# Performance work log

Measured on AMD Instinct MI355X. Metric: run time of the kernel, lower is better.

The kernel has to match this reference:

```python
import jax, jax.numpy as jnp
import numpy as np

NEG_LARGE = -2.0**32 + 1.0


def setup_inputs() -> dict:
    key = jax.random.key(0)
    ks = jax.random.split(key, 8)
    B, L, D = 2048, 200, 64  # D = embedding_dim, features are 2D wide
    H1, H2 = 80, 40
    queries = jax.random.normal(ks[0], (B, 2 * D), dtype=jnp.float32)
    user_behaviors = jax.random.normal(ks[1], (B, L, 2 * D), dtype=jnp.float32)
    masks = jax.random.randint(ks[2], (B, L), 0, 2, dtype=jnp.int32)
    s = 1.0 / np.sqrt(8 * D)
    w1 = jax.random.uniform(ks[3], (8 * D, H1), minval=-s, maxval=s, dtype=jnp.float32)
    b1 = jnp.zeros((H1,), jnp.float32)
    s2 = 1.0 / np.sqrt(H1)
    w2 = jax.random.uniform(ks[4], (H1, H2), minval=-s2, maxval=s2, dtype=jnp.float32)
    b2 = jnp.zeros((H2,), jnp.float32)
    s3 = 1.0 / np.sqrt(H2)
    w3 = jax.random.uniform(ks[5], (H2, 1), minval=-s3, maxval=s3, dtype=jnp.float32)
    b3 = jnp.zeros((1,), jnp.float32)
    return {"queries": queries, "user_behaviors": user_behaviors, "masks": masks,
            "w1": w1, "b1": b1, "w2": w2, "b2": b2, "w3": w3, "b3": b3}


def reference(queries, user_behaviors, masks, w1, b1, w2, b2, w3, b3):
    B, L, twoD = user_behaviors.shape
    q = jnp.broadcast_to(queries[:, None, :], (B, L, twoD))  # (B, L, 2D)
    feats = jnp.concatenate([q, user_behaviors, q - user_behaviors,
                             q * user_behaviors], axis=-1)  # (B, L, 8D)
    h = jax.nn.sigmoid(jnp.einsum('blf,fh->blh', feats, w1) + b1)
    h = jax.nn.sigmoid(jnp.einsum('blh,hk->blk', h, w2) + b2)
    scores = jnp.einsum('blk,ko->blo', h, w3) + b3  # (B, L, 1)
    valid = (masks != 0)[:, :, None]
    scores = jnp.where(valid, scores, NEG_LARGE)
    attn = jax.nn.softmax(scores, axis=1)  # (B, L, 1)
    return jnp.sum(attn * user_behaviors, axis=1)  # (B, 2D)
```

## Files before the change

### kernel.cpp

```cpp
#include <hip/hip_runtime.h>
#include <cstddef>


#define L_   200
#define D2_  128

typedef __attribute__((ext_vector_type(8))) short bf16x8;
typedef __attribute__((ext_vector_type(4))) float f32x4;
typedef __attribute__((ext_vector_type(4))) unsigned int u32x4;

__device__ __forceinline__ float sigmoidf_(float x) { return 1.0f / (1.0f + __expf(-x)); }

__device__ __forceinline__ unsigned int f2bf_(float x) {
  unsigned int u = __float_as_uint(x);
  return (u + 0x7fffu + ((u >> 16) & 1u)) >> 16;
}
__device__ __forceinline__ unsigned int pk2_(float a, float b) {
  return f2bf_(a) | (f2bf_(b) << 16);
}

extern "C" __global__ void __launch_bounds__(256, 3)
din_attn_kernel(const float* __restrict__ queries,
                const float* __restrict__ ub,
                const int*   __restrict__ masks,
                const float* __restrict__ w1,
                const float* __restrict__ b1,
                const float* __restrict__ w2,
                const float* __restrict__ b2,
                const float* __restrict__ w3,
                float* __restrict__ out)
{
  __shared__ __align__(16) char pool[39936];
  __shared__ __align__(16) char w2f[9216];
  __shared__ __align__(16) float q_s[128];
  __shared__ __align__(16) float qt_s[80];
  __shared__ __align__(16) float b2_s[48];
  __shared__ __align__(16) float w3_s[48];
  __shared__ __align__(16) float scores_s[208];
  __shared__ float red_s[8];

  const int b    = blockIdx.x;
  const int t    = threadIdx.x;
  const int wave = t >> 6;
  const int lane = t & 63;

  const float* ubbase = ub + (size_t)b * L_ * D2_;
  const float4* ub4base = (const float4*)ubbase;

  if (t < 128) q_s[t] = queries[(size_t)b * D2_ + t];
  if (t < 48) {
    b2_s[t] = (t < 40) ? b2[t] : 0.0f;
    w3_s[t] = (t < 40) ? w3[t] : 0.0f;
  }
  __syncthreads();

  if (t < 80) {
    float acc = b1[t];
    #pragma unroll 4
    for (int k = 0; k < 128; ++k)
      acc += q_s[k] * (w1[k * 80 + t] + w1[(256 + k) * 80 + t]);
    qt_s[t] = acc;
  }

  {
    u32x4* dst = (u32x4*)(pool + 13312);
    #pragma unroll
    for (int i = 0; i < 5; ++i) {
      int s = i * 256 + t;
      int n = s & 15, kg = (s >> 4) & 3, g = s >> 6;
      int kc = g / 5, nt = g - kc * 5;
      int h = nt * 16 + n, k0 = kc * 32 + kg * 8;
      float wv[8];
      #pragma unroll
      for (int j = 0; j < 8; ++j) {
        int k = k0 + j;
        wv[j] = w1[(128 + k) * 80 + h] - w1[(256 + k) * 80 + h]
              + q_s[k] * w1[(384 + k) * 80 + h];
      }
      u32x4 v = { pk2_(wv[0], wv[1]), pk2_(wv[2], wv[3]),
                  pk2_(wv[4], wv[5]), pk2_(wv[6], wv[7]) };
      dst[s] = v;
    }
  }

  {
    u32x4* dst = (u32x4*)w2f;
    #pragma unroll
    for (int i = 0; i < 3; ++i) {
      int s = i * 256 + t;
      if (s < 576) {
        int n = s & 15, g = s >> 4;
        int nt2 = g / 12, kg = g - nt2 * 12;
        int j = nt2 * 16 + n;
        u32x4 v = { 0u, 0u, 0u, 0u };
        if (j < 40 && kg < 10) {
          int k0 = kg * 8;
          float e0 = w2[(k0 + 0) * 40 + j], e1 = w2[(k0 + 1) * 40 + j];
          float e2 = w2[(k0 + 2) * 40 + j], e3 = w2[(k0 + 3) * 40 + j];
          float e4 = w2[(k0 + 4) * 40 + j], e5 = w2[(k0 + 5) * 40 + j];
          float e6 = w2[(k0 + 6) * 40 + j], e7 = w2[(k0 + 7) * 40 + j];
          v = (u32x4){ pk2_(e0, e1), pk2_(e2, e3), pk2_(e4, e5), pk2_(e6, e7) };
        }
        dst[s] = v;
      }
    }
  }

  f32x4 acc[17];
  #pragma unroll
  for (int i = 0; i < 17; ++i) acc[i] = (f32x4){0.f, 0.f, 0.f, 0.f};

  const bf16x8* Af = (const bf16x8*)pool;
  const bf16x8* Bf = (const bf16x8*)(pool + 13312);

  for (int kc = 0; kc < 4; ++kc) {
    u32x4* dst = (u32x4*)pool;
    #pragma unroll
    for (int i = 0; i < 4; ++i) {
      int s = i * 256 + t;
      if (s < 832) {
        int m = s & 15, kg = (s >> 4) & 3, mt = s >> 6;
        int l = mt * 16 + m;
        u32x4 v = { 0u, 0u, 0u, 0u };
        if (l < L_) {
          const float4* src = (const float4*)(ubbase + (size_t)l * D2_ + kc * 32 + kg * 8);
          float4 u0 = src[0], u1 = src[1];
          v = (u32x4){ pk2_(u0.x, u0.y), pk2_(u0.z, u0.w), pk2_(u1.x, u1.y), pk2_(u1.z, u1.w) };
        }
        dst[s] = v;
      }
    }
    __syncthreads();

    #pragma unroll
    for (int i = 0; i < 17; ++i) {
      int tt = i * 4 + wave;
      if (tt < 65) {
        int mt = tt / 5, nt = tt - mt * 5;
        bf16x8 av = Af[mt * 64 + lane];
        bf16x8 bv = Bf[(kc * 5 + nt) * 64 + lane];
        acc[i] = __builtin_amdgcn_mfma_f32_16x16x32_bf16(av, bv, acc[i], 0, 0, 0);
      }
    }
    __syncthreads();
  }

  {
    u32x4* pz = (u32x4*)pool;
    #pragma unroll
    for (int s = 0; s < 2; ++s) {
      int idx = s * 256 + t;
      if (idx < 416) {
        int mt = idx >> 5, off = idx & 31;
        pz[(mt * 12 + 10) * 16 + off] = (u32x4){ 0u, 0u, 0u, 0u };
      }
    }
    unsigned short* hv = (unsigned short*)pool;
    const int n = lane & 15, rg = lane >> 4;
    #pragma unroll
    for (int i = 0; i < 17; ++i) {
      int tt = i * 4 + wave;
      if (tt < 65) {
        int mt = tt / 5, nt = tt - mt * 5;
        int h = nt * 16 + n;
        int kg = h >> 3, hb = h & 7;
        float qtv = qt_s[h];
        #pragma unroll
        for (int r = 0; r < 4; ++r) {
          float x = acc[i][r] + qtv;
          hv[((mt * 12 + kg) * 16 + rg * 4 + r) * 8 + hb] = (unsigned short)f2bf_(sigmoidf_(x));
        }
      }
    }
  }
  __syncthreads();

  f32x4 acc2[4][3];
  #pragma unroll
  for (int i = 0; i < 4; ++i)
    #pragma unroll
    for (int n2 = 0; n2 < 3; ++n2) acc2[i][n2] = (f32x4){0.f, 0.f, 0.f, 0.f};

  {
    const bf16x8* hvf = (const bf16x8*)pool;
    const bf16x8* w2ff = (const bf16x8*)w2f;
    #pragma unroll
    for (int i = 0; i < 4; ++i) {
      int mt = wave + i * 4;
      if (mt < 13) {
        #pragma unroll
        for (int ks = 0; ks < 3; ++ks) {
          bf16x8 av = hvf[mt * 192 + ks * 64 + lane];
          #pragma unroll
          for (int n2 = 0; n2 < 3; ++n2) {
            bf16x8 bv = w2ff[n2 * 192 + ks * 64 + lane];
            acc2[i][n2] = __builtin_amdgcn_mfma_f32_16x16x32_bf16(av, bv, acc2[i][n2], 0, 0, 0);
          }
        }
      }
    }
  }

  {
    const int n = lane & 15, rg = lane >> 4;
    #pragma unroll
    for (int i = 0; i < 4; ++i) {
      int mt = wave + i * 4;
      if (mt < 13) {
        #pragma unroll
        for (int r = 0; r < 4; ++r) {
          float s = 0.0f;
          #pragma unroll
          for (int n2 = 0; n2 < 3; ++n2) {
            int j = n2 * 16 + n;
            s += sigmoidf_(acc2[i][n2][r] + b2_s[j]) * w3_s[j];
          }
          s += __shfl_xor(s, 1, 64);
          s += __shfl_xor(s, 2, 64);
          s += __shfl_xor(s, 4, 64);
          s += __shfl_xor(s, 8, 64);
          int l = mt * 16 + rg * 4 + r;
          if (n == 0 && l < L_) scores_s[l] = s;
        }
      }
    }
  }
  __syncthreads();

  float sval = -INFINITY;
  if (t < L_) {
    int mv = masks[(size_t)b * L_ + t];
    sval = mv ? scores_s[t] : -4294967295.0f;
  }
  float m = sval;
  #pragma unroll
  for (int o = 32; o > 0; o >>= 1) m = fmaxf(m, __shfl_xor(m, o, 64));
  if (lane == 0) red_s[wave] = m;
  __syncthreads();
  m = fmaxf(fmaxf(red_s[0], red_s[1]), fmaxf(red_s[2], red_s[3]));
  float e = (t < L_) ? __expf(sval - m) : 0.0f;
  float ssum = e;
  #pragma unroll
  for (int o = 32; o > 0; o >>= 1) ssum += __shfl_xor(ssum, o, 64);
  if (lane == 0) red_s[4 + wave] = ssum;
  __syncthreads();
  ssum = red_s[4] + red_s[5] + red_s[6] + red_s[7];
  float attn = e / ssum;
  __syncthreads();
  if (t < L_) scores_s[t] = attn;
  __syncthreads();

  {
    float* wsum = (float*)pool;
    int d4 = t & 31;
    int lg = t >> 5;
    float4 o = make_float4(0.f, 0.f, 0.f, 0.f);
    #pragma unroll 5
    for (int l = lg; l < L_; l += 8) {
      float w = scores_s[l];
      float4 v = ub4base[l * 32 + d4];
      o.x += w * v.x; o.y += w * v.y; o.z += w * v.z; o.w += w * v.w;
    }
    *(float4*)(wsum + lg * 136 + d4 * 4) = o;
    __syncthreads();
    if (t < 128) {
      float s = 0.0f;
      #pragma unroll
      for (int g = 0; g < 8; ++g) s += wsum[g * 136 + t];
      out[(size_t)b * 128 + t] = s;
    }
  }
}

extern "C" void kernel_launch(void* const* d_in, const int* in_sizes, int n_in,
                              void* d_out, int out_size, void* d_ws, size_t ws_size,
                              hipStream_t stream) {
  const float* queries = (const float*)d_in[0];
  const float* ub      = (const float*)d_in[1];
  const int*   masks   = (const int*)d_in[2];
  const float* w1      = (const float*)d_in[3];
  const float* b1      = (const float*)d_in[4];
  const float* w2      = (const float*)d_in[5];
  const float* b2      = (const float*)d_in[6];
  const float* w3      = (const float*)d_in[7];
  float* out = (float*)d_out;

  const int B = in_sizes[0] / D2_;
  din_attn_kernel<<<B, 256, 0, stream>>>(queries, ub, masks, w1, b1, w2, b2, w3, out);
}
```

Before: 391.2 us.

## Split q*ub term into a second MFMA, vectorize the w1 weight prep

The old code folded the q*ub product into a per-batch B matrix built with scalar loads. The new code builds a batch-independent B with K=256 from float4 loads of w1, and forms the u*q product on the A side as a second bf16 MFMA per tile. The qt projection is parallelized across 160 threads with a partial-sum reduction, and shared memory is reorganized into two regions. This doubles the MFMA count and the A-side LDS writes, and the launch bound drops from 3 to 2 blocks per CU, which may reduce occupancy.

```diff
diff --git a/kernel.cpp b/kernel.cpp
--- a/kernel.cpp
+++ b/kernel.cpp
@@ -18,8 +18,11 @@
 __device__ __forceinline__ unsigned int pk2_(float a, float b) {
   return f2bf_(a) | (f2bf_(b) << 16);
 }
-
-extern "C" __global__ void __launch_bounds__(256, 3)
+__device__ __forceinline__ float f4get(const float4& v, int c) {
+  return c == 0 ? v.x : c == 1 ? v.y : c == 2 ? v.z : v.w;
+}
+
+extern "C" __global__ void __launch_bounds__(256, 2)
 din_attn_kernel(const float* __restrict__ queries,
                 const float* __restrict__ ub,
                 const int*   __restrict__ masks,
@@ -30,8 +33,9 @@
                 const float* __restrict__ w3,
                 float* __restrict__ out)
 {
-  __shared__ __align__(16) char pool[39936];
-  __shared__ __align__(16) char w2f[9216];
+  __shared__ __align__(16) char region0[40960];
+  __shared__ __align__(16) char region1[26624];
+  __shared__ __align__(16) float qtp[640];
   __shared__ __align__(16) float q_s[128];
   __shared__ __align__(16) float qt_s[80];
   __shared__ __align__(16) float b2_s[48];
@@ -54,37 +58,149 @@
   }
   __syncthreads();
 
+  {
+    u32x4* Bdst = (u32x4*)region0;
+    #pragma unroll
+    for (int i = 0; i < 3; ++i) {
+      int u = i * 256 + t;
+      if (u < 640) {
+        int h4 = u % 20;
+        int r  = u / 20;
+        int kg = r & 3, kc = r >> 2;
+        int k0 = kc * 32 + kg * 8;
+        int hb = h4 * 4;
+        float4 v[8];
+        if (kc < 4) {
+          #pragma unroll
+          for (int j = 0; j < 8; ++j) {
+            float4 p = *(const float4*)(w1 + (128 + k0 + j) * 80 + hb);
+            float4 c = *(const float4*)(w1 + (256 + k0 + j) * 80 + hb);
+            v[j] = make_float4(p.x - c.x, p.y - c.y, p.z - c.z, p.w - c.w);
+          }
+        } else {
+          int k0p = k0 - 128;
+          #pragma unroll
+          for (int j = 0; j < 8; ++j)
+            v[j] = *(const float4*)(w1 + (384 + k0p + j) * 80 + hb);
+        }
+        int nt = hb >> 4, n = hb & 15;
+        int sbase = ((kc * 5 + nt) * 4 + kg) * 16 + n;
+        #pragma unroll
+        for (int hh = 0; hh < 4; ++hh) {
+          u32x4 w = { pk2_(f4get(v[0], hh), f4get(v[1], hh)),
+                      pk2_(f4get(v[2], hh), f4get(v[3], hh)),
+                      pk2_(f4get(v[4], hh), f4get(v[5], hh)),
+                      pk2_(f4get(v[6], hh), f4get(v[7], hh)) };
+          Bdst[sbase + hh] = w;
+        }
+      }
+    }
+  }
+
+  if (t < 160) {
+    int h4 = t % 20, kseg = t / 20;
+    int k0 = kseg * 16, hb = h4 * 4;
+    float4 accq = make_float4(0.f, 0.f, 0.f, 0.f);
+    #pragma unroll
+    for (int k = 0; k < 16; ++k) {
+      float qk = q_s[k0 + k];
+      float4 a = *(const float4*)(w1 + (k0 + k) * 80 + hb);
+      float4 c = *(const float4*)(w1 + (256 + k0 + k) * 80 + hb);
+      accq.x += qk * (a.x + c.x); accq.y += qk * (a.y + c.y);
+      accq.z += qk * (a.z + c.z); accq.w += qk * (a.w + c.w);
+    }
+    *(float4*)(qtp + (kseg * 20 + h4) * 4) = accq;
+  }
+  __syncthreads();
   if (t < 80) {
-    float acc = b1[t];
-    #pragma unroll 4
-    for (int k = 0; k < 128; ++k)
-      acc += q_s[k] * (w1[k * 80 + t] + w1[(256 + k) * 80 + t]);
-    qt_s[t] = acc;
-  }
-
-  {
-    u32x4* dst = (u32x4*)(pool + 13312);
-    #pragma unroll
-    for (int i = 0; i < 5; ++i) {
+    float accq = b1[t];
+    int h4 = t >> 2, hh = t & 3;
+    #pragma unroll
+    for (int ks = 0; ks < 8; ++ks) accq += qtp[(ks * 20 + h4) * 4 + hh];
+    qt_s[t] = accq;
+  }
+
+  f32x4 acc[17];
+  #pragma unroll
+  for (int i = 0; i < 17; ++i) acc[i] = (f32x4){0.f, 0.f, 0.f, 0.f};
+
+  const bf16x8* Bf = (const bf16x8*)region0;
+  const bf16x8* Ap = (const bf16x8*)region1;
+  const bf16x8* Am = (const bf16x8*)(region1 + 13312);
+
+  for (int kc = 0; kc < 4; ++kc) {
+    u32x4* dp = (u32x4*)region1;
+    u32x4* dm = (u32x4*)(region1 + 13312);
+    #pragma unroll
+    for (int i = 0; i < 4; ++i) {
       int s = i * 256 + t;
-      int n = s & 15, kg = (s >> 4) & 3, g = s >> 6;
-      int kc = g / 5, nt = g - kc * 5;
-      int h = nt * 16 + n, k0 = kc * 32 + kg * 8;
-      float wv[8];
-      #pragma unroll
-      for (int j = 0; j < 8; ++j) {
-        int k = k0 + j;
-        wv[j] = w1[(128 + k) * 80 + h] - w1[(256 + k) * 80 + h]
-              + q_s[k] * w1[(384 + k) * 80 + h];
-      }
-      u32x4 v = { pk2_(wv[0], wv[1]), pk2_(wv[2], wv[3]),
-                  pk2_(wv[4], wv[5]), pk2_(wv[6], wv[7]) };
-      dst[s] = v;
-    }
-  }
-
-  {
-    u32x4* dst = (u32x4*)w2f;
+      if (s < 832) {
+        int m = s & 15, kg = (s >> 4) & 3, mt = s >> 6;
+        int l = mt * 16 + m;
+        u32x4 vp = { 0u, 0u, 0u, 0u }, vm = { 0u, 0u, 0u, 0u };
+        if (l < L_) {
+          const float4* src = (const float4*)(ubbase + (size_t)l * D2_ + kc * 32 + kg * 8);
+          float4 u0 = src[0], u1 = src[1];
+          const float4* qq = (const float4*)(q_s + kc * 32 + kg * 8);
+          float4 q0 = qq[0], q1 = qq[1];
+          vp = (u32x4){ pk2_(u0.x, u0.y), pk2_(u0.z, u0.w),
+                        pk2_(u1.x, u1.y), pk2_(u1.z, u1.w) };
+          vm = (u32x4){ pk2_(u0.x * q0.x, u0.y * q0.y), pk2_(u0.z * q0.z, u0.w * q0.w),
+                        pk2_(u1.x * q1.x, u1.y * q1.y), pk2_(u1.z * q1.z, u1.w * q1.w) };
+        }
+        dp[s] = vp; dm[s] = vm;
+      }
+    }
+    __syncthreads();
+
+    #pragma unroll
+    for (int i = 0; i < 17; ++i) {
+      int tt = i * 4 + wave;
+      if (tt < 65) {
+        int mt = tt / 5, nt = tt - mt * 5;
+        bf16x8 avp = Ap[mt * 64 + lane];
+        bf16x8 avm = Am[mt * 64 + lane];
+        bf16x8 bvp = Bf[(kc * 5 + nt) * 64 + lane];
+        bf16x8 bvm = Bf[((kc + 4) * 5 + nt) * 64 + lane];
+        acc[i] = __builtin_amdgcn_mfma_f32_16x16x32_bf16(avp, bvp, acc[i], 0, 0, 0);
+        acc[i] = __builtin_amdgcn_mfma_f32_16x16x32_bf16(avm, bvm, acc[i], 0, 0, 0);
+      }
+    }
+    __syncthreads();
+  }
+
+  {
+    u32x4* pz = (u32x4*)region0;
+    #pragma unroll
+    for (int s = 0; s < 2; ++s) {
+      int idx = s * 256 + t;
+      if (idx < 416) {
+        int mt = idx >> 5, off = idx & 31;
+        pz[(mt * 12 + 10) * 16 + off] = (u32x4){ 0u, 0u, 0u, 0u };
+      }
+    }
+    unsigned short* hv = (unsigned short*)region0;
+    const int n = lane & 15, rg = lane >> 4;
+    #pragma unroll
+    for (int i = 0; i < 17; ++i) {
+      int tt = i * 4 + wave;
+      if (tt < 65) {
+        int mt = tt / 5, nt = tt - mt * 5;
+        int h = nt * 16 + n;
+        int kg = h >> 3, hb = h & 7;
+        float qtv = qt_s[h];
+        #pragma unroll
+        for (int r = 0; r < 4; ++r) {
+          float x = acc[i][r] + qtv;
+          hv[((mt * 12 + kg) * 16 + rg * 4 + r) * 8 + hb] =
+              (unsigned short)f2bf_(sigmoidf_(x));
+        }
+      }
+    }
+  }
+
+  {
+    u32x4* dst = (u32x4*)region1;
     #pragma unroll
     for (int i = 0; i < 3; ++i) {
       int s = i * 256 + t;
@@ -105,74 +221,6 @@
       }
     }
   }
-
-  f32x4 acc[17];
-  #pragma unroll
-  for (int i = 0; i < 17; ++i) acc[i] = (f32x4){0.f, 0.f, 0.f, 0.f};
-
-  const bf16x8* Af = (const bf16x8*)pool;
-  const bf16x8* Bf = (const bf16x8*)(pool + 13312);
-
-  for (int kc = 0; kc < 4; ++kc) {
-    u32x4* dst = (u32x4*)pool;
-    #pragma unroll
-    for (int i = 0; i < 4; ++i) {
-      int s = i * 256 + t;
-      if (s < 832) {
-        int m = s & 15, kg = (s >> 4) & 3, mt = s >> 6;
-        int l = mt * 16 + m;
-        u32x4 v = { 0u, 0u, 0u, 0u };
-        if (l < L_) {
-          const float4* src = (const float4*)(ubbase + (size_t)l * D2_ + kc * 32 + kg * 8);
-          float4 u0 = src[0], u1 = src[1];
-          v = (u32x4){ pk2_(u0.x, u0.y), pk2_(u0.z, u0.w), pk2_(u1.x, u1.y), pk2_(u1.z, u1.w) };
-        }
-        dst[s] = v;
-      }
-    }
-    __syncthreads();
-
-    #pragma unroll
-    for (int i = 0; i < 17; ++i) {
-      int tt = i * 4 + wave;
-      if (tt < 65) {
-        int mt = tt / 5, nt = tt - mt * 5;
-        bf16x8 av = Af[mt * 64 + lane];
-        bf16x8 bv = Bf[(kc * 5 + nt) * 64 + lane];
-        acc[i] = __builtin_amdgcn_mfma_f32_16x16x32_bf16(av, bv, acc[i], 0, 0, 0);
-      }
-    }
-    __syncthreads();
-  }
-
-  {
-    u32x4* pz = (u32x4*)pool;
-    #pragma unroll
-    for (int s = 0; s < 2; ++s) {
-      int idx = s * 256 + t;
-      if (idx < 416) {
-        int mt = idx >> 5, off = idx & 31;
-        pz[(mt * 12 + 10) * 16 + off] = (u32x4){ 0u, 0u, 0u, 0u };
-      }
-    }
-    unsigned short* hv = (unsigned short*)pool;
-    const int n = lane & 15, rg = lane >> 4;
-    #pragma unroll
-    for (int i = 0; i < 17; ++i) {
-      int tt = i * 4 + wave;
-      if (tt < 65) {
-        int mt = tt / 5, nt = tt - mt * 5;
-        int h = nt * 16 + n;
-        int kg = h >> 3, hb = h & 7;
-        float qtv = qt_s[h];
-        #pragma unroll
-        for (int r = 0; r < 4; ++r) {
-          float x = acc[i][r] + qtv;
-          hv[((mt * 12 + kg) * 16 + rg * 4 + r) * 8 + hb] = (unsigned short)f2bf_(sigmoidf_(x));
-        }
-      }
-    }
-  }
   __syncthreads();
 
   f32x4 acc2[4][3];
@@ -182,8 +230,8 @@
     for (int n2 = 0; n2 < 3; ++n2) acc2[i][n2] = (f32x4){0.f, 0.f, 0.f, 0.f};
 
   {
-    const bf16x8* hvf = (const bf16x8*)pool;
-    const bf16x8* w2ff = (const bf16x8*)w2f;
+    const bf16x8* hvf = (const bf16x8*)region0;
+    const bf16x8* w2ff = (const bf16x8*)region1;
     #pragma unroll
     for (int i = 0; i < 4; ++i) {
       int mt = wave + i * 4;
@@ -251,7 +299,7 @@
   __syncthreads();
 
   {
-    float* wsum = (float*)pool;
+    float* wsum = (float*)region0;
     int d4 = t & 31;
     int lg = t >> 5;
     float4 o = make_float4(0.f, 0.f, 0.f, 0.f);
```

Result: no change. 394.4 us (+0.8%).
